# Optimization experiments

Hardware: AMD Instinct MI355X
Metric: run time of the kernel (lower is better)

## Reference

```python
import jax, jax.numpy as jnp
import numpy as np

EPS = 1e-5

def _ln(x, s, b):
    mu = jnp.mean(x, axis=-1, keepdims=True)
    var = jnp.mean((x - mu) ** 2, axis=-1, keepdims=True)
    return (x - mu) * jax.lax.rsqrt(var + EPS) * s + b

def _gelu(x):
    return jax.nn.gelu(x, approximate=False)


def setup_inputs() -> dict:
    key = jax.random.key(0)
    ks = jax.random.split(key, 24)
    B, L, C, E, T, FC, MULT = 8, 4096, 128, 1048576, 512, 32, 2
    N = B * L
    inp = {}
    inp['feats'] = jax.random.normal(ks[0], (N, C), jnp.float32)
    inp['edge_index'] = jax.random.randint(ks[1], (2, E), 0, N, jnp.int32)
    inp['edge_attr'] = jax.random.normal(ks[2], (E, 2), jnp.float32) * 0.05  # relative coords
    inp['t'] = jax.random.normal(ks[3], (B, T), jnp.float32)
    inp['norm_vec'] = jnp.ones((N, 1), jnp.float32)
    # LayerNorms
    inp['ln1_scale'] = jnp.ones((C,), jnp.float32); inp['ln1_bias'] = jnp.zeros((C,), jnp.float32)
    inp['ln2_scale'] = jnp.ones((C,), jnp.float32); inp['ln2_bias'] = jnp.zeros((C,), jnp.float32)
    # time mlps: GELU -> Linear(T, 2C)
    sc = lambda k, sh: jax.random.normal(k, sh, jnp.float32) / np.sqrt(sh[0])
    inp['tmlp1_w'] = sc(ks[4], (T, 2 * C)); inp['tmlp1_b'] = jnp.zeros((2 * C,), jnp.float32)
    inp['tmlp2_w'] = sc(ks[5], (T, 2 * C)); inp['tmlp2_b'] = jnp.zeros((2 * C,), jnp.float32)
    # continuous-kernel MLP: 2 -> FC -> FC -> C (depthwise weights)
    inp['ker_w1'] = sc(ks[6], (2, FC)); inp['ker_b1'] = jnp.zeros((FC,), jnp.float32)
    inp['ker_w2'] = sc(ks[7], (FC, FC)); inp['ker_b2'] = jnp.zeros((FC,), jnp.float32)
    inp['ker_w3'] = sc(ks[8], (FC, C)); inp['ker_b3'] = jnp.zeros((C,), jnp.float32)
    inp['conv_bias'] = jnp.zeros((C,), jnp.float32)
    # feedforward mlp: C -> mult*C -> C
    inp['mlp_w1'] = sc(ks[9], (C, MULT * C)); inp['mlp_b1'] = jnp.zeros((MULT * C,), jnp.float32)
    inp['mlp_w2'] = sc(ks[10], (MULT * C, C)); inp['mlp_b2'] = jnp.zeros((C,), jnp.float32)
    return inp


def reference(feats, edge_index, edge_attr, t, norm_vec,
              ln1_scale, ln1_bias, ln2_scale, ln2_bias,
              tmlp1_w, tmlp1_b, tmlp2_w, tmlp2_b,
              ker_w1, ker_b1, ker_w2, ker_b2, ker_w3, ker_b3, conv_bias,
              mlp_w1, mlp_b1, mlp_w2, mlp_b2):
    N, C = feats.shape
    B = t.shape[0]
    q = N // B  # nodes per image

    def modulate(f, ln_s, ln_b, tw, tb):
        h = _ln(f, ln_s, ln_b)
        tm = _gelu(t) @ tw + tb                       # [B, 2C]
        tm = jnp.repeat(tm, q, axis=0)                # [(B q), 2C]
        scale, shift = jnp.split(tm, 2, axis=-1)
        return h * (1.0 + scale) + shift

    # pre-conv modulation
    h = modulate(feats, ln1_scale, ln1_bias, tmlp1_w, tmlp1_b)

    # continuous conv: per-edge depthwise kernel from edge_attr
    k = _gelu(edge_attr @ ker_w1 + ker_b1)
    k = _gelu(k @ ker_w2 + ker_b2)
    w = k @ ker_w3 + ker_b3                           # [E, C]
    src, dst = edge_index[0], edge_index[1]
    msg = w * h[src]                                  # gather + weight  [E, C]
    h = jax.ops.segment_sum(msg, dst, num_segments=N) + conv_bias
    h = h / norm_vec                                  # tg_div normalization

    x = feats + h                                     # residual 1

    # post-conv modulation + MLP
    h2 = modulate(x, ln2_scale, ln2_bias, tmlp2_w, tmlp2_b)
    h2 = _gelu(h2 @ mlp_w1 + mlp_b1) @ mlp_w2 + mlp_b2
    return x + h2                                     # residual 2
```

## Files before the change

kernel.cpp:

```cpp
#include <hip/hip_runtime.h>
#include <hip/hip_bf16.h>

#define C_DIM 128
#define TWO_C 256
#define FC    32
#define T_DIM 512

typedef unsigned int   u32;
typedef unsigned short u16;
typedef unsigned long long u64;
typedef short bf16x8 __attribute__((ext_vector_type(8)));
typedef float f32x4  __attribute__((ext_vector_type(4)));

__device__ __forceinline__ float fast_rcp(float x) {
    return __builtin_amdgcn_rcpf(x);
}
__device__ __forceinline__ float gelu_f(float x) {
    float a = fabsf(x);
    float p = 1.0f + a * (0.19685352f + a * (0.11519450f +
              a * (3.4364302e-4f + a * 0.019527027f)));
    float d  = fast_rcp(p);
    float d2 = d * d;
    float d4 = d2 * d2;
    float s = 0.5f * x;
    return s + s * copysignf(1.0f - d4, x);
}
__device__ __forceinline__ u32 f2bf_bits(float x) {
    u32 u = __float_as_uint(x);
    return (u + 0x7fffu + ((u >> 16) & 1u)) >> 16;
}
__device__ __forceinline__ u32 pack_bf2(float lo, float hi) {
    __hip_bfloat162 p = __float22bfloat162_rn(make_float2(lo, hi));
    u32 r; __builtin_memcpy(&r, &p, 4); return r;
}
__device__ __forceinline__ float bf2f(u16 v) {
    return __uint_as_float((u32)v << 16);
}
__device__ __forceinline__ int hperm(int c) {
    return ((c >> 5) << 5) + ((c & 15) << 1) + ((c >> 4) & 1);
}

__global__ __launch_bounds__(256) void k_tmod(const float* __restrict__ t,
                                              const float* __restrict__ tw1,
                                              const float* __restrict__ tb1,
                                              float* __restrict__ tm1,
                                              const float* __restrict__ tw2,
                                              const float* __restrict__ tb2,
                                              float* __restrict__ tm2) {
    const float* tw = blockIdx.y ? tw2 : tw1;
    const float* tb = blockIdx.y ? tb2 : tb1;
    float*       tm = blockIdx.y ? tm2 : tm1;
    __shared__ float gt[T_DIM];
    int b = blockIdx.x;
    for (int k = threadIdx.x; k < T_DIM; k += 256)
        gt[k] = gelu_f(t[(size_t)b * T_DIM + k]);
    __syncthreads();
    int j = threadIdx.x;
    float acc = tb[j];
    for (int k = 0; k < T_DIM; ++k)
        acc += gt[k] * tw[(size_t)k * TWO_C + j];
    tm[(size_t)b * TWO_C + j] = acc;
}

template <bool BF16OUT, bool ZROW, bool PERM>
__global__ __launch_bounds__(C_DIM) void k_mod(const float* __restrict__ in,
                                               const float* __restrict__ lns,
                                               const float* __restrict__ lnb,
                                               const float* __restrict__ tm,
                                               void* __restrict__ outp, int q, int N) {
    int n = blockIdx.x, c = threadIdx.x;
    if (ZROW && n == N) {
        ((u16*)outp)[(size_t)N * C_DIM + c] = 0;
        return;
    }
    size_t o = (size_t)n * C_DIM + c;
    float v = in[o];
    float s1 = v, s2 = v * v;
#pragma unroll
    for (int off = 32; off > 0; off >>= 1) {
        s1 += __shfl_down(s1, off);
        s2 += __shfl_down(s2, off);
    }
    __shared__ float red[4];
    if ((c & 63) == 0) { red[(c >> 6) * 2] = s1; red[(c >> 6) * 2 + 1] = s2; }
    __syncthreads();
    float mean = (red[0] + red[2]) * (1.0f / C_DIM);
    float ex2  = (red[1] + red[3]) * (1.0f / C_DIM);
    float r    = rsqrtf(ex2 - mean * mean + 1e-5f);
    int b = n / q;
    float scale = tm[(size_t)b * TWO_C + c];
    float shift = tm[(size_t)b * TWO_C + C_DIM + c];
    float h = (v - mean) * r * lns[c] + lnb[c];
    float res = h * (1.0f + scale) + shift;
    if (BF16OUT) {
        int idx = PERM ? hperm(c) : c;
        ((u16*)outp)[(size_t)n * C_DIM + idx] = (u16)f2bf_bits(res);
    } else {
        ((float*)outp)[o] = res;
    }
}

__global__ void k_hist(const int* __restrict__ dst, int* __restrict__ cnt,
                       int* __restrict__ rank, int E) {
    int e = blockIdx.x * 256 + threadIdx.x;
    if (e < E) rank[e] = atomicAdd(&cnt[dst[e]], 1);
}

__global__ __launch_bounds__(1024) void k_scan_bsum(const int* __restrict__ cnt,
                                                    u64* __restrict__ bsum, int N) {
    __shared__ u64 red[1024];
    int t = threadIdx.x;
    int idx = blockIdx.x * 1024 + t;
    int v = (idx < N) ? cnt[idx] : 0;
    red[t] = (u64)(u32)v | ((u64)(u32)((v + 15) >> 4) << 32);
    __syncthreads();
#pragma unroll
    for (int off = 512; off > 0; off >>= 1) {
        if (t < off) red[t] += red[t + off];
        __syncthreads();
    }
    if (t == 0) bsum[blockIdx.x] = red[0];
}

__global__ __launch_bounds__(1024) void k_scan_btop(u64* __restrict__ bsum,
                                                    int* __restrict__ Ttot, int nb) {
    __shared__ u64 tot[1024];
    int t = threadIdx.x;
    u64 v = (t < nb) ? bsum[t] : 0ull;
    tot[t] = v;
    __syncthreads();
    for (int off = 1; off < 1024; off <<= 1) {
        u64 a = (t >= off) ? tot[t - off] : 0ull;
        __syncthreads();
        tot[t] += a;
        __syncthreads();
    }
    if (t < nb) bsum[t] = tot[t] - v;
    if (t == 1023) Ttot[0] = (int)(tot[1023] >> 32);
}

__global__ __launch_bounds__(1024) void k_scan_final(const int* __restrict__ cnt,
                                                     const u64* __restrict__ bsum,
                                                     int* __restrict__ startn,
                                                     int4* __restrict__ tinfo, int N) {
    __shared__ u64 tot[1024];
    int t = threadIdx.x;
    int idx = blockIdx.x * 1024 + t;
    int v = (idx < N) ? cnt[idx] : 0;
    u64 pk = (u64)(u32)v | ((u64)(u32)((v + 15) >> 4) << 32);
    tot[t] = pk;
    __syncthreads();
    for (int off = 1; off < 1024; off <<= 1) {
        u64 a = (t >= off) ? tot[t - off] : 0ull;
        __syncthreads();
        tot[t] += a;
        __syncthreads();
    }
    if (idx >= N) return;
    u64 ex = tot[t] - pk + bsum[blockIdx.x];
    int rd = (int)(ex & 0xffffffffull);
    int rt = (int)(ex >> 32);
    startn[idx] = rd;
    int nt = (v + 15) >> 4;
    int e = rd + v;
    for (int k = 0; k < nt; ++k)
        tinfo[rt + k] = make_int4(idx, rd + 16 * k, e, 0);
}

__global__ void k_sed(const int* __restrict__ ei,
                      const int* __restrict__ rank,
                      const int* __restrict__ startn,
                      const float* __restrict__ ea,
                      uint2* __restrict__ sed2, int E) {
    int e = blockIdx.x * 256 + threadIdx.x;
    if (e >= E) return;
    int pos = startn[ei[E + e]] + rank[e];
    float2 av = ((const float2*)ea)[e];
    uint2 v;
    v.x = pack_bf2(av.x, av.y);
    v.y = (u32)ei[e];
    sed2[pos] = v;
}

__global__ __launch_bounds__(256) void k_edgek2s(
        const uint2* __restrict__ sed2,
        const float* __restrict__ w1, const float* __restrict__ b1,
        const u16* __restrict__ w2kf, const float* __restrict__ b2,
        u32* __restrict__ k2h, int E) {
    int l = threadIdx.x & 63, wv = threadIdx.x >> 6;
    int lr = l & 15, g = l >> 4;
    int wbase = blockIdx.x * 256 + wv * 64;

    bf16x8 wb0 = *(const bf16x8*)(w2kf + (size_t)l * 8);
    bf16x8 wb1 = *(const bf16x8*)(w2kf + (size_t)(64 + l) * 8);
    f32x4 bi0, bi1;
    {
        float v0 = b2[lr], v1 = b2[16 + lr];
        bi0[0] = v0; bi0[1] = v0; bi0[2] = v0; bi0[3] = v0;
        bi1[0] = v1; bi1[1] = v1; bi1[2] = v1; bi1[3] = v1;
    }
    float w1x[8], w1y[8], b1v[8];
#pragma unroll
    for (int j = 0; j < 8; ++j) {
        w1x[j] = w1[8 * g + j];
        w1y[j] = w1[FC + 8 * g + j];
        b1v[j] = b1[8 * g + j];
    }
#pragma unroll
    for (int c = 0; c < 4; ++c) {
        int cb = wbase + 16 * c;
        int pA = cb + lr;
        float ax = 0.f, ay = 0.f;
        if (pA < E) {
            u32 pr = sed2[pA].x;
            ax = bf2f((u16)(pr & 0xffffu));
            ay = bf2f((u16)(pr >> 16));
        }
        union { u32 w[4]; bf16x8 v; } au;
#pragma unroll
        for (int m = 0; m < 4; ++m) {
            float v0 = gelu_f(fmaf(ax, w1x[2 * m],     fmaf(ay, w1y[2 * m],     b1v[2 * m])));
            float v1 = gelu_f(fmaf(ax, w1x[2 * m + 1], fmaf(ay, w1y[2 * m + 1], b1v[2 * m + 1])));
            au.w[m] = pack_bf2(v0, v1);
        }
        f32x4 d0 = __builtin_amdgcn_mfma_f32_16x16x32_bf16(au.v, wb0, bi0, 0, 0, 0);
        f32x4 d1 = __builtin_amdgcn_mfma_f32_16x16x32_bf16(au.v, wb1, bi1, 0, 0, 0);
#pragma unroll
        for (int r = 0; r < 4; ++r) {
            int pD = cb + 4 * g + r;
            if (pD < E) {
                u32 pk = pack_bf2(gelu_f(d0[r]), gelu_f(d1[r]));
                k2h[(size_t)pD * 16 + lr] = pk;
            }
        }
    }
}

#define PREP_TOT (32768 + 32768 + 4096 + 1024)
__global__ __launch_bounds__(256) void k_prep(const float* __restrict__ mw1,
                                              const float* __restrict__ mw2,
                                              const float* __restrict__ kw3,
                                              const float* __restrict__ kw2,
                                              u16* __restrict__ w1f,
                                              u16* __restrict__ w2f,
                                              u16* __restrict__ w3f,
                                              u16* __restrict__ w2kf) {
    int t = blockIdx.x * 256 + threadIdx.x;
    if (t < 32768) {
        int j = t & 7, l = (t >> 3) & 63, f = t >> 9;
        int ks = f & 3, nt = f >> 2;
        int k = ks * 32 + ((l >> 4) << 3) + j, n = nt * 16 + (l & 15);
        w1f[t] = (u16)f2bf_bits(mw1[(size_t)k * TWO_C + n]);
    } else if (t < 65536) {
        int t2 = t - 32768;
        int j = t2 & 7, l = (t2 >> 3) & 63, f = t2 >> 9;
        int ks = f & 7, nt = f >> 3;
        int k = ks * 32 + ((l >> 4) << 3) + j, n = nt * 16 + (l & 15);
        w2f[t2] = (u16)f2bf_bits(mw2[(size_t)k * C_DIM + n]);
    } else if (t < 69632) {
        int t3 = t - 65536;
        int j = t3 & 7, l = (t3 >> 3) & 63, nt = t3 >> 9;
        int kk = ((l >> 4) << 3) + j;
        int k = (kk >> 1) + ((kk & 1) << 4);
        int n = nt * 16 + (l & 15);
        w3f[t3] = (u16)f2bf_bits(kw3[(size_t)k * C_DIM + n]);
    } else if (t < PREP_TOT) {
        int t4 = t - 69632;
        int j = t4 & 7, l = (t4 >> 3) & 63, nt = t4 >> 9;
        int kk = ((l >> 4) << 3) + j;
        int n = nt * 16 + (l & 15);
        w2kf[t4] = (u16)f2bf_bits(kw2[(size_t)kk * FC + n]);
    }
}

__global__ __launch_bounds__(256, 5) void k_conv4(
        const u16* __restrict__ h_mod,
        const int* __restrict__ Ttot,
        const int4* __restrict__ tinfo,
        const u32* __restrict__ k2h,
        const uint2* __restrict__ sed2,
        const u16* __restrict__ w3f, const float* __restrict__ kb3,
        float* __restrict__ xbuf, int N) {
    int l = threadIdx.x & 63, wv = threadIdx.x >> 6;
    int lr = l & 15, g = l >> 4;

    bf16x8 w3b[8];
#pragma unroll
    for (int nt = 0; nt < 8; ++nt)
        w3b[nt] = *(const bf16x8*)(w3f + ((size_t)nt * 64 + l) * 8);
    float b3c[8];
#pragma unroll
    for (int nt = 0; nt < 8; ++nt) b3c[nt] = kb3[nt * 16 + lr];
    const f32x4 zc = {0.f, 0.f, 0.f, 0.f};
    const u32* h32 = (const u32*)h_mod;

    int T = Ttot[0];
    int nw = gridDim.x * 4;
#pragma unroll 1
    for (int t = blockIdx.x * 4 + wv; t < T; t += nw) {
        int4 ti = tinfo[t];
        int n = ti.x, p0 = ti.y, e = ti.z;
        int pa = p0 + lr;
        bf16x8 a = {0, 0, 0, 0, 0, 0, 0, 0};
        if (pa < e) a = *(const bf16x8*)(k2h + (size_t)pa * 16 + g * 4);
        int srcv[4];
#pragma unroll
        for (int r = 0; r < 4; ++r) {
            int pp = p0 + 4 * g + r;
            srcv[r] = (pp < e) ? (int)sed2[pp].y : N;
        }
        const u32* h0p = h32 + (size_t)srcv[0] * 64 + lr;
        const u32* h1p = h32 + (size_t)srcv[1] * 64 + lr;
        const u32* h2p = h32 + (size_t)srcv[2] * 64 + lr;
        const u32* h3p = h32 + (size_t)srcv[3] * 64 + lr;
        float acc[8];
#pragma unroll
        for (int j = 0; j < 4; ++j) {
            f32x4 w0 = __builtin_amdgcn_mfma_f32_16x16x32_bf16(a, w3b[2 * j],     zc, 0, 0, 0);
            f32x4 w1 = __builtin_amdgcn_mfma_f32_16x16x32_bf16(a, w3b[2 * j + 1], zc, 0, 0, 0);
            u32 u0 = h0p[j * 16], u1 = h1p[j * 16], u2 = h2p[j * 16], u3 = h3p[j * 16];
            float l0 = __uint_as_float(u0 << 16), h0 = __uint_as_float(u0 & 0xffff0000u);
            float l1 = __uint_as_float(u1 << 16), h1 = __uint_as_float(u1 & 0xffff0000u);
            float l2 = __uint_as_float(u2 << 16), h2 = __uint_as_float(u2 & 0xffff0000u);
            float l3 = __uint_as_float(u3 << 16), h3 = __uint_as_float(u3 & 0xffff0000u);
            acc[2 * j]     = w0[0] * l0 + w0[1] * l1 + w0[2] * l2 + w0[3] * l3
                           + b3c[2 * j] * (l0 + l1 + l2 + l3);
            acc[2 * j + 1] = w1[0] * h0 + w1[1] * h1 + w1[2] * h2 + w1[3] * h3
                           + b3c[2 * j + 1] * (h0 + h1 + h2 + h3);
        }
#pragma unroll
        for (int nt = 0; nt < 8; ++nt) {
            acc[nt] += __shfl_xor(acc[nt], 16, 64);
            acc[nt] += __shfl_xor(acc[nt], 32, 64);
        }
        float v0 = (g == 0) ? acc[0] : (g == 1) ? acc[2] : (g == 2) ? acc[4] : acc[6];
        float v1 = (g == 0) ? acc[1] : (g == 1) ? acc[3] : (g == 2) ? acc[5] : acc[7];
        float* row = xbuf + (size_t)n * C_DIM + 32 * g + lr;
        atomicAdd(row, v0);
        atomicAdd(row + 16, v1);
    }
}

__global__ __launch_bounds__(256) void k_ffn3(const float* __restrict__ feats,
                                              const float* __restrict__ xbuf,
                                              const float* __restrict__ cbias,
                                              const float* __restrict__ normv,
                                              const float* __restrict__ tm2,
                                              const float* __restrict__ ln2s,
                                              const float* __restrict__ ln2b,
                                              const u16* __restrict__ w1f,
                                              const float* __restrict__ b1,
                                              const u16* __restrict__ w2f,
                                              const float* __restrict__ b2,
                                              float* __restrict__ out, int q) {
    __shared__ u16 xmt[2048];
    __shared__ float xt[16][128];
    __shared__ u16 sm[4096];
    __shared__ float red2[2][4];
    int tid = threadIdx.x;
    int n0 = blockIdx.x * 16;

    {
        int gi = tid >> 7, c = tid & 127;
#pragma unroll 1
        for (int it = 0; it < 8; ++it) {
            int rA = 2 * it + gi;
            int n = n0 + rA;
            size_t o = (size_t)n * C_DIM + c;
            float v = feats[o] + (xbuf[o] + cbias[c]) * fast_rcp(normv[n]);
            float s1 = v, s2 = v * v;
#pragma unroll
            for (int off = 32; off > 0; off >>= 1) {
                s1 += __shfl_down(s1, off);
                s2 += __shfl_down(s2, off);
            }
            if ((c & 63) == 0) {
                red2[gi][(c >> 6) * 2] = s1;
                red2[gi][(c >> 6) * 2 + 1] = s2;
            }
            __syncthreads();
            float mean = (red2[gi][0] + red2[gi][2]) * (1.0f / C_DIM);
            float ex2  = (red2[gi][1] + red2[gi][3]) * (1.0f / C_DIM);
            float r    = rsqrtf(ex2 - mean * mean + 1e-5f);
            int b = n / q;
            float scale = tm2[(size_t)b * TWO_C + c];
            float shift = tm2[(size_t)b * TWO_C + C_DIM + c];
            float h = (v - mean) * r * ln2s[c] + ln2b[c];
            float res = h * (1.0f + scale) + shift;
            int byte = rA * 256 + ((c * 2) ^ ((rA & 7) << 4));
            xmt[byte >> 1] = (u16)f2bf_bits(res);
            xt[rA][c] = v;
            __syncthreads();
        }
    }

    int w = tid >> 6, l = tid & 63;
    int lr = l & 15, g = l >> 4;

    bf16x8 a[4];
#pragma unroll
    for (int ks = 0; ks < 4; ++ks) {
        int byte = lr * 256 + ((ks * 64 + g * 16) ^ ((lr & 7) << 4));
        a[ks] = *(const bf16x8*)((const char*)xmt + byte);
    }
    f32x4 acc[4];
#pragma unroll
    for (int i = 0; i < 4; ++i) {
        int nt = w + 4 * i;
        float bv = b1[nt * 16 + lr];
        acc[i][0] = bv; acc[i][1] = bv; acc[i][2] = bv; acc[i][3] = bv;
#pragma unroll
        for (int ks = 0; ks < 4; ++ks) {
            bf16x8 bfr = *(const bf16x8*)(w1f + ((size_t)(nt * 4 + ks) * 64 + l) * 8);
            acc[i] = __builtin_amdgcn_mfma_f32_16x16x32_bf16(a[ks], bfr, acc[i], 0, 0, 0);
        }
    }
#pragma unroll
    for (int i = 0; i < 4; ++i) {
        int nt = w + 4 * i;
#pragma unroll
        for (int r = 0; r < 4; ++r) {
            int row = 4 * g + r, col = nt * 16 + lr;
            int byte = row * 512 + ((col * 2) ^ ((row & 7) << 4));
            sm[byte >> 1] = (u16)f2bf_bits(gelu_f(acc[i][r]));
        }
    }
    __syncthreads();
    f32x4 acc2[2];
#pragma unroll
    for (int i = 0; i < 2; ++i) {
        int nt2 = 2 * w + i;
        float bv = b2[nt2 * 16 + lr];
        acc2[i][0] = bv; acc2[i][1] = bv; acc2[i][2] = bv; acc2[i][3] = bv;
    }
#pragma unroll
    for (int ks = 0; ks < 8; ++ks) {
        int byte = lr * 512 + ((ks * 64 + g * 16) ^ ((lr & 7) << 4));
        bf16x8 a2 = *(const bf16x8*)(sm + (byte >> 1));
#pragma unroll
        for (int i = 0; i < 2; ++i) {
            int nt2 = 2 * w + i;
            bf16x8 bfr = *(const bf16x8*)(w2f + ((size_t)(nt2 * 8 + ks) * 64 + l) * 8);
            acc2[i] = __builtin_amdgcn_mfma_f32_16x16x32_bf16(a2, bfr, acc2[i], 0, 0, 0);
        }
    }
#pragma unroll
    for (int i = 0; i < 2; ++i) {
        int nt2 = 2 * w + i;
#pragma unroll
        for (int r = 0; r < 4; ++r) {
            size_t o = (size_t)(n0 + 4 * g + r) * C_DIM + nt2 * 16 + lr;
            out[o] = xt[4 * g + r][nt2 * 16 + lr] + acc2[i][r];
        }
    }
}

__global__ __launch_bounds__(256) void k_edge_atomic(
        const int* __restrict__ ei, const float* __restrict__ ea,
        const float* __restrict__ w1, const float* __restrict__ b1,
        const float* __restrict__ w2, const float* __restrict__ b2,
        const float* __restrict__ w3, const float* __restrict__ b3,
        const u16* __restrict__ h_mod, float* __restrict__ xacc, int E) {
    int e = blockIdx.x * 256 + threadIdx.x;
    if (e >= E) return;
    int src = ei[e], dst = ei[E + e];
    float ax = ea[(size_t)e * 2], ay = ea[(size_t)e * 2 + 1];
    float k1[FC];
#pragma unroll
    for (int i = 0; i < FC; ++i) k1[i] = gelu_f(ax * w1[i] + ay * w1[FC + i] + b1[i]);
    float k2v[FC];
#pragma unroll
    for (int j = 0; j < FC; ++j) {
        float acc = b2[j];
#pragma unroll
        for (int i = 0; i < FC; ++i) acc += k1[i] * w2[i * FC + j];
        k2v[j] = gelu_f(acc);
    }
    const u16* hrow = h_mod + (size_t)src * C_DIM;
    float* orow = xacc + (size_t)dst * C_DIM;
    for (int c = 0; c < C_DIM; ++c) {
        float wv = b3[c];
#pragma unroll
        for (int j = 0; j < FC; ++j) wv += k2v[j] * w3[j * C_DIM + c];
        atomicAdd(&orow[c], wv * bf2f(hrow[hperm(c)]));
    }
}

extern "C" void kernel_launch(void* const* d_in, const int* in_sizes, int n_in,
                              void* d_out, int out_size, void* d_ws, size_t ws_size,
                              hipStream_t stream) {
    const float* feats = (const float*)d_in[0];
    const int*   ei    = (const int*)d_in[1];
    const float* ea    = (const float*)d_in[2];
    const float* t     = (const float*)d_in[3];
    const float* normv = (const float*)d_in[4];
    const float* ln1s  = (const float*)d_in[5];
    const float* ln1b  = (const float*)d_in[6];
    const float* ln2s  = (const float*)d_in[7];
    const float* ln2b  = (const float*)d_in[8];
    const float* tw1   = (const float*)d_in[9];
    const float* tb1   = (const float*)d_in[10];
    const float* tw2   = (const float*)d_in[11];
    const float* tb2   = (const float*)d_in[12];
    const float* kw1   = (const float*)d_in[13];
    const float* kb1   = (const float*)d_in[14];
    const float* kw2   = (const float*)d_in[15];
    const float* kb2   = (const float*)d_in[16];
    const float* kw3   = (const float*)d_in[17];
    const float* kb3   = (const float*)d_in[18];
    const float* cbias = (const float*)d_in[19];
    const float* mw1   = (const float*)d_in[20];
    const float* mb1   = (const float*)d_in[21];
    const float* mw2   = (const float*)d_in[22];
    const float* mb2   = (const float*)d_in[23];
    float* out = (float*)d_out;

    const int N = in_sizes[0] / C_DIM;
    const int E = in_sizes[1] / 2;
    const int B = in_sizes[3] / T_DIM;
    const int q = N / B;
    const int nb = (N + 1023) / 1024;

    char* wp = (char*)d_ws;
    auto alloc = [&](size_t bytes) -> char* {
        char* p = wp; wp += (bytes + 255) & ~(size_t)255; return p;
    };
    float* tm1    = (float*)alloc((size_t)B * TWO_C * 4);
    float* tm2    = (float*)alloc((size_t)B * TWO_C * 4);
    u16*   h_mod  = (u16*)alloc(((size_t)N + 1) * C_DIM * 2);
    u16*   w1f    = (u16*)alloc((size_t)C_DIM * TWO_C * 2);
    u16*   w2f    = (u16*)alloc((size_t)TWO_C * C_DIM * 2);
    u16*   w3f    = (u16*)alloc((size_t)FC * C_DIM * 2);
    u16*   w2kf   = (u16*)alloc((size_t)FC * FC * 2);
    int*   cnt    = (int*)alloc(((size_t)N + 1) * 4);
    int*   startn = (int*)alloc((size_t)N * 4);
    int*   rank   = (int*)alloc((size_t)E * 4);
    u64*   bsum   = (u64*)alloc(((size_t)nb + 1) * 8);
    int*   Ttot   = (int*)alloc(256);
    int4*  tinfo  = (int4*)alloc(((size_t)E / 16 + N + 64) * 16);
    float* xbuf   = (float*)alloc((size_t)N * C_DIM * 4);
    uint2* sed2   = (uint2*)alloc(((size_t)E + 16) * 8);
    size_t fixed = (size_t)(wp - (char*)d_ws);
    bool can_sort = ws_size >= fixed + ((size_t)E + 16) * 64;
    u32* k2h = (u32*)alloc(((size_t)E + 16) * 64);

    const int eb = (E + 255) / 256;

    k_tmod<<<dim3(B, 2), 256, 0, stream>>>(t, tw1, tb1, tm1, tw2, tb2, tm2);
    k_mod<true, true, true><<<N + 1, C_DIM, 0, stream>>>(feats, ln1s, ln1b, tm1,
                                                         h_mod, q, N);
    k_prep<<<(PREP_TOT + 255) / 256, 256, 0, stream>>>(mw1, mw2, kw3, kw2,
                                                       w1f, w2f, w3f, w2kf);
    hipMemsetAsync(xbuf, 0, (size_t)N * C_DIM * 4, stream);

    if (can_sort) {
        hipMemsetAsync(cnt, 0, ((size_t)N + 1) * 4, stream);
        k_hist<<<eb, 256, 0, stream>>>(ei + E, cnt, rank, E);
        k_scan_bsum<<<nb, 1024, 0, stream>>>(cnt, bsum, N);
        k_scan_btop<<<1, 1024, 0, stream>>>(bsum, Ttot, nb);
        k_scan_final<<<nb, 1024, 0, stream>>>(cnt, bsum, startn, tinfo, N);
        k_sed<<<eb, 256, 0, stream>>>(ei, rank, startn, ea, sed2, E);
        k_edgek2s<<<eb, 256, 0, stream>>>(sed2, kw1, kb1, w2kf, kb2, k2h, E);
        k_conv4<<<3072, 256, 0, stream>>>(h_mod, Ttot, tinfo, k2h, sed2,
                                          w3f, kb3, xbuf, N);
    } else {
        k_edge_atomic<<<eb, 256, 0, stream>>>(ei, ea, kw1, kb1, kw2, kb2, kw3, kb3,
                                              h_mod, xbuf, E);
    }

    k_ffn3<<<N / 16, 256, 0, stream>>>(feats, xbuf, cbias, normv, tm2, ln2s, ln2b,
                                       w1f, mb1, w2f, mb2, out, q);
}
```

Baseline: 223.9 us.

## Merge front-end prep kernels and memsets into one launch; retune conv occupancy

Combines the time-MLP, weight-format prep, count clearing and xbuf zeroing into a single k_front launch, so several small kernel launches and two memsets are replaced by one grid. The modulation branch of k_front is a dead stub (nbMod=0) and the separate k_mod launch is kept. Separately, launch bounds for k_edgek2s and k_conv4 are raised to 8 waves per SIMD and k_conv4's grid grows from 3072 to 4096 blocks. The higher occupancy target may force register spills in the conv kernels.

```diff
diff --git a/kernel.cpp b/kernel.cpp
--- a/kernel.cpp
+++ b/kernel.cpp
@@ -5,6 +5,7 @@
 #define TWO_C 256
 #define FC    32
 #define T_DIM 512
+#define PREP_TOT (32768 + 32768 + 4096 + 1024)
 
 typedef unsigned int   u32;
 typedef unsigned short u16;
@@ -40,26 +41,119 @@
     return ((c >> 5) << 5) + ((c & 15) << 1) + ((c >> 4) & 1);
 }
 
-__global__ __launch_bounds__(256) void k_tmod(const float* __restrict__ t,
-                                              const float* __restrict__ tw1,
-                                              const float* __restrict__ tb1,
-                                              float* __restrict__ tm1,
-                                              const float* __restrict__ tw2,
-                                              const float* __restrict__ tb2,
-                                              float* __restrict__ tm2) {
-    const float* tw = blockIdx.y ? tw2 : tw1;
-    const float* tb = blockIdx.y ? tb2 : tb1;
-    float*       tm = blockIdx.y ? tm2 : tm1;
-    __shared__ float gt[T_DIM];
-    int b = blockIdx.x;
-    for (int k = threadIdx.x; k < T_DIM; k += 256)
-        gt[k] = gelu_f(t[(size_t)b * T_DIM + k]);
-    __syncthreads();
-    int j = threadIdx.x;
-    float acc = tb[j];
-    for (int k = 0; k < T_DIM; ++k)
-        acc += gt[k] * tw[(size_t)k * TWO_C + j];
-    tm[(size_t)b * TWO_C + j] = acc;
+__global__ __launch_bounds__(256) void k_front(
+        const float* __restrict__ feats,
+        const float* __restrict__ ln1s, const float* __restrict__ ln1b,
+        const float* __restrict__ t,
+        const float* __restrict__ tw1, const float* __restrict__ tb1,
+        const float* __restrict__ tw2, const float* __restrict__ tb2,
+        const float* __restrict__ mw1, const float* __restrict__ mw2,
+        const float* __restrict__ kw3, const float* __restrict__ kw2,
+        float* __restrict__ tm1, float* __restrict__ tm2,
+        u16* __restrict__ h_mod,
+        u16* __restrict__ w1f, u16* __restrict__ w2f,
+        u16* __restrict__ w3f, u16* __restrict__ w2kf,
+        int* __restrict__ cnt, float* __restrict__ xbuf,
+        int q, int N, int B,
+        int nbMod, int nbPrep, int nbCnt, int nbXb) {
+    int bid = blockIdx.x, tid = threadIdx.x;
+
+    if (bid < nbMod) {
+        __shared__ float red2[2][4];
+        int gi = tid >> 7, c = tid & 127;
+        int n = 2 * bid + gi;
+        if (n > N) return;
+        if (n == N) { h_mod[(size_t)N * C_DIM + c] = 0; return; }
+        size_t o = (size_t)n * C_DIM + c;
+        float v = feats[o];
+        float s1 = v, s2 = v * v;
+#pragma unroll
+        for (int off = 32; off > 0; off >>= 1) {
+            s1 += __shfl_down(s1, off);
+            s2 += __shfl_down(s2, off);
+        }
+        if ((c & 63) == 0) {
+            red2[gi][(c >> 6) * 2] = s1;
+            red2[gi][(c >> 6) * 2 + 1] = s2;
+        }
+        __syncthreads();
+        float mean = (red2[gi][0] + red2[gi][2]) * (1.0f / C_DIM);
+        float ex2  = (red2[gi][1] + red2[gi][3]) * (1.0f / C_DIM);
+        float r    = rsqrtf(ex2 - mean * mean + 1e-5f);
+        int b = n / q;
+        float scale = tm1  == nullptr ? 0.f : 0.f;
+        (void)scale;
+        float sc = __ldg(&tw1[0]) * 0.f; (void)sc;
+        float scl = ((const float*)tm1)[0] * 0.f; (void)scl;
+        (void)r; (void)b; (void)v; (void)o;
+        return;
+    }
+    bid -= nbMod;
+
+    if (bid < 2 * B) {
+        int y = bid >= B;
+        int b = y ? bid - B : bid;
+        const float* tw = y ? tw2 : tw1 == tm1 ? tw1 : (y ? tw2 : tw1);
+        (void)tw;
+        const float* twp = y ? tw2 : tw1;
+        const float* tbp = y ? tb2 : tb1;
+        float*       tmp = y ? tm2 : tm1;
+        __shared__ float gt[T_DIM];
+        for (int k = tid; k < T_DIM; k += 256)
+            gt[k] = gelu_f(t[(size_t)b * T_DIM + k]);
+        __syncthreads();
+        float acc = tbp[tid];
+        for (int k = 0; k < T_DIM; ++k)
+            acc += gt[k] * twp[(size_t)k * TWO_C + tid];
+        tmp[(size_t)b * TWO_C + tid] = acc;
+        return;
+    }
+    bid -= 2 * B;
+
+    if (bid < nbPrep) {
+        int tt = bid * 256 + tid;
+        if (tt < 32768) {
+            int j = tt & 7, l = (tt >> 3) & 63, f = tt >> 9;
+            int ks = f & 3, nt = f >> 2;
+            int k = ks * 32 + ((l >> 4) << 3) + j, n = nt * 16 + (l & 15);
+            w1f[tt] = (u16)f2bf_bits(mw1[(size_t)k * TWO_C + n]);
+        } else if (tt < 65536) {
+            int t2 = tt - 32768;
+            int j = t2 & 7, l = (t2 >> 3) & 63, f = t2 >> 9;
+            int ks = f & 7, nt = f >> 3;
+            int k = ks * 32 + ((l >> 4) << 3) + j, n = nt * 16 + (l & 15);
+            w2f[t2] = (u16)f2bf_bits(mw2[(size_t)k * C_DIM + n]);
+        } else if (tt < 69632) {
+            int t3 = tt - 65536;
+            int j = t3 & 7, l = (t3 >> 3) & 63, nt = t3 >> 9;
+            int kk = ((l >> 4) << 3) + j;
+            int k = (kk >> 1) + ((kk & 1) << 4);
+            int n = nt * 16 + (l & 15);
+            w3f[t3] = (u16)f2bf_bits(kw3[(size_t)k * C_DIM + n]);
+        } else if (tt < PREP_TOT) {
+            int t4 = tt - 69632;
+            int j = t4 & 7, l = (t4 >> 3) & 63, nt = t4 >> 9;
+            int kk = ((l >> 4) << 3) + j;
+            int n = nt * 16 + (l & 15);
+            w2kf[t4] = (u16)f2bf_bits(kw2[(size_t)kk * FC + n]);
+        }
+        return;
+    }
+    bid -= nbPrep;
+
+    if (bid < nbCnt) {
+        int i = bid * 256 + tid;
+        if (i <= N) cnt[i] = 0;
+        return;
+    }
+    bid -= nbCnt;
+
+    if (bid < nbXb) {
+        size_t i = ((size_t)bid * 256 + tid) * 4;
+        if (i < (size_t)N * C_DIM)
+            *(float4*)(xbuf + i) = make_float4(0.f, 0.f, 0.f, 0.f);
+        return;
+    }
 }
 
 template <bool BF16OUT, bool ZROW, bool PERM>
@@ -182,7 +276,7 @@
     sed2[pos] = v;
 }
 
-__global__ __launch_bounds__(256) void k_edgek2s(
+__global__ __launch_bounds__(256, 8) void k_edgek2s(
         const uint2* __restrict__ sed2,
         const float* __restrict__ w1, const float* __restrict__ b1,
         const u16* __restrict__ w2kf, const float* __restrict__ b2,
@@ -236,44 +330,7 @@
     }
 }
 
-#define PREP_TOT (32768 + 32768 + 4096 + 1024)
-__global__ __launch_bounds__(256) void k_prep(const float* __restrict__ mw1,
-                                              const float* __restrict__ mw2,
-                                              const float* __restrict__ kw3,
-                                              const float* __restrict__ kw2,
-                                              u16* __restrict__ w1f,
-                                              u16* __restrict__ w2f,
-                                              u16* __restrict__ w3f,
-                                              u16* __restrict__ w2kf) {
-    int t = blockIdx.x * 256 + threadIdx.x;
-    if (t < 32768) {
-        int j = t & 7, l = (t >> 3) & 63, f = t >> 9;
-        int ks = f & 3, nt = f >> 2;
-        int k = ks * 32 + ((l >> 4) << 3) + j, n = nt * 16 + (l & 15);
-        w1f[t] = (u16)f2bf_bits(mw1[(size_t)k * TWO_C + n]);
-    } else if (t < 65536) {
-        int t2 = t - 32768;
-        int j = t2 & 7, l = (t2 >> 3) & 63, f = t2 >> 9;
-        int ks = f & 7, nt = f >> 3;
-        int k = ks * 32 + ((l >> 4) << 3) + j, n = nt * 16 + (l & 15);
-        w2f[t2] = (u16)f2bf_bits(mw2[(size_t)k * C_DIM + n]);
-    } else if (t < 69632) {
-        int t3 = t - 65536;
-        int j = t3 & 7, l = (t3 >> 3) & 63, nt = t3 >> 9;
-        int kk = ((l >> 4) << 3) + j;
-        int k = (kk >> 1) + ((kk & 1) << 4);
-        int n = nt * 16 + (l & 15);
-        w3f[t3] = (u16)f2bf_bits(kw3[(size_t)k * C_DIM + n]);
-    } else if (t < PREP_TOT) {
-        int t4 = t - 69632;
-        int j = t4 & 7, l = (t4 >> 3) & 63, nt = t4 >> 9;
-        int kk = ((l >> 4) << 3) + j;
-        int n = nt * 16 + (l & 15);
-        w2kf[t4] = (u16)f2bf_bits(kw2[(size_t)kk * FC + n]);
-    }
-}
-
-__global__ __launch_bounds__(256, 5) void k_conv4(
+__global__ __launch_bounds__(256, 8) void k_conv4(
         const u16* __restrict__ h_mod,
         const int* __restrict__ Ttot,
         const int4* __restrict__ tinfo,
@@ -546,22 +603,26 @@
 
     const int eb = (E + 255) / 256;
 
-    k_tmod<<<dim3(B, 2), 256, 0, stream>>>(t, tw1, tb1, tm1, tw2, tb2, tm2);
+    const int nbPrep = (PREP_TOT + 255) / 256;
+    const int nbCnt  = (N + 1 + 255) / 256;
+    const int nbXb   = (N * (C_DIM / 4) + 255) / 256;
+    const int nbFront = 2 * B + nbPrep + nbCnt + nbXb;
+
+    k_front<<<nbFront, 256, 0, stream>>>(feats, ln1s, ln1b, t, tw1, tb1, tw2, tb2,
+                                         mw1, mw2, kw3, kw2, tm1, tm2, h_mod,
+                                         w1f, w2f, w3f, w2kf, cnt, xbuf,
+                                         q, N, B, 0, nbPrep, nbCnt, nbXb);
     k_mod<true, true, true><<<N + 1, C_DIM, 0, stream>>>(feats, ln1s, ln1b, tm1,
                                                          h_mod, q, N);
-    k_prep<<<(PREP_TOT + 255) / 256, 256, 0, stream>>>(mw1, mw2, kw3, kw2,
-                                                       w1f, w2f, w3f, w2kf);
-    hipMemsetAsync(xbuf, 0, (size_t)N * C_DIM * 4, stream);
 
     if (can_sort) {
-        hipMemsetAsync(cnt, 0, ((size_t)N + 1) * 4, stream);
         k_hist<<<eb, 256, 0, stream>>>(ei + E, cnt, rank, E);
         k_scan_bsum<<<nb, 1024, 0, stream>>>(cnt, bsum, N);
         k_scan_btop<<<1, 1024, 0, stream>>>(bsum, Ttot, nb);
         k_scan_final<<<nb, 1024, 0, stream>>>(cnt, bsum, startn, tinfo, N);
         k_sed<<<eb, 256, 0, stream>>>(ei, rank, startn, ea, sed2, E);
         k_edgek2s<<<eb, 256, 0, stream>>>(sed2, kw1, kb1, w2kf, kb2, k2h, E);
-        k_conv4<<<3072, 256, 0, stream>>>(h_mod, Ttot, tinfo, k2h, sed2,
+        k_conv4<<<4096, 256, 0, stream>>>(h_mod, Ttot, tinfo, k2h, sed2,
                                           w3f, kb3, xbuf, N);
     } else {
         k_edge_atomic<<<eb, 256, 0, stream>>>(ei, ea, kw1, kb1, kw2, kb2, kw3, kb3,
```

Result: slower. 292.1 us (+30.5%).
